# Kernel optimization log

Measured on AMD Instinct MI355X. Metric: run time of the kernel, lower is better.

Reference implementation:

```python
import jax, jax.numpy as jnp
import numpy as np


def _gcn_layer(x, W, b, row, col, num_nodes):
    # x: [N, F_in]; W: [F_in, F_out]; row/col: [E2] (with self-loops appended)
    xw = x @ W  # [N, F_out]
    ones = jnp.ones(row.shape[0], dtype=xw.dtype)
    deg = jax.ops.segment_sum(ones, col, num_segments=num_nodes)  # in-degree incl. self-loop
    dinv = jnp.where(deg > 0, jax.lax.rsqrt(deg), 0.0)
    norm = dinv[row] * dinv[col]  # [E2]
    msg = xw[row] * norm[:, None]  # gather + per-edge scale
    out = jax.ops.segment_sum(msg, col, num_segments=num_nodes)  # scatter-add to targets
    return out + b


def setup_inputs() -> dict:
    key = jax.random.key(0)
    k1, k2, k3, k4, k5 = jax.random.split(key, 5)
    N, E, F_in, F_hid = 100000, 640000, 128, 128
    x = jax.random.normal(k1, (N, F_in), dtype=jnp.float32)
    edge_index = jax.random.randint(k2, (2, E), 0, N, dtype=jnp.int64)
    # Glorot-style init like PyG GCNConv
    s1 = (6.0 / (F_in + F_hid)) ** 0.5
    W1 = jax.random.uniform(k3, (F_in, F_hid), jnp.float32, -s1, s1)
    b1 = jnp.zeros((F_hid,), jnp.float32)
    s2 = (6.0 / (F_hid + F_hid)) ** 0.5
    W2 = jax.random.uniform(k4, (F_hid, F_hid), jnp.float32, -s2, s2)
    b2 = jnp.zeros((F_hid,), jnp.float32)
    return {"x": x, "edge_index": edge_index, "W1": W1, "b1": b1, "W2": W2, "b2": b2}


def reference(x, edge_index, W1, b1, W2, b2):
    N = x.shape[0]
    # GCN adds self-loops before symmetric normalization (add_self_loops=True default)
    self_idx = jnp.arange(N, dtype=edge_index.dtype)
    row = jnp.concatenate([edge_index[0], self_idx])
    col = jnp.concatenate([edge_index[1], self_idx])
    h = _gcn_layer(x, W1, b1, row, col, N)
    h = jax.nn.relu(h)
    # dropout is identity in eval mode (training=False)
    out = _gcn_layer(h, W2, b2, row, col, N)
    return out
```

## Files before the change

kernel.cpp:

```cpp
#include <hip/hip_runtime.h>
#include <cstdint>
#include <cstddef>


typedef unsigned int u32;
typedef unsigned short u16;
typedef __attribute__((ext_vector_type(8))) short short8;
typedef __attribute__((ext_vector_type(4))) float f32x4;

__device__ __forceinline__ float bf2f(u32 lo16) {
  union { u32 u; float f; } c; c.u = lo16 << 16; return c.f;
}
__device__ __forceinline__ u32 f2bf(float f) {
  union { float f; u32 u; } c; c.f = f;
  return (c.u + 0x7fffu + ((c.u >> 16) & 1u)) >> 16;
}

__global__ __launch_bounds__(256) void zero_wt_kernel(
    const float* __restrict__ W1, const float* __restrict__ W2,
    u16* __restrict__ Wt1, u16* __restrict__ Wt2,
    u16* __restrict__ s1, u16* __restrict__ hp,
    int* __restrict__ cnt, int N) {
  int gt = blockIdx.x * 256 + threadIdx.x;
  if (gt < N) cnt[gt] = 0;
  if (gt < 32768) {
    const float* W = (gt < 16384) ? W1 : W2;
    u16* Wt = (gt < 16384) ? Wt1 : Wt2;
    int idx = gt & 16383;
    Wt[(idx & 127) * 128 + (idx >> 7)] = (u16)f2bf(W[idx]);
  }
  if (gt < 16) {
    ((uint4*)(s1 + (size_t)N * 128))[gt] = make_uint4(0, 0, 0, 0);
    ((uint4*)(hp + (size_t)N * 128))[gt] = make_uint4(0, 0, 0, 0);
  }
}

__global__ __launch_bounds__(256) void count_kernel(
    const int* __restrict__ cols, const int* __restrict__ rows,
    int* __restrict__ cnt, int E, int N) {
  int e = blockIdx.x * 256 + threadIdx.x;
  if (e >= E) return;
  int c = cols[e];
  int r = rows[e];
  if ((unsigned)c >= (unsigned)N || (unsigned)r >= (unsigned)N) return;
  atomicAdd(&cnt[c], 1);
}

__global__ __launch_bounds__(256) void scan1_kernel(
    const int* __restrict__ cnt, int* __restrict__ rowptr,
    int* __restrict__ bsum, float* __restrict__ dinv, int N) {
  __shared__ int sd[256];
  int t = threadIdx.x;
  int base = blockIdx.x * 1024 + t * 4;
  int c0 = (base + 0 < N) ? cnt[base + 0] : 0;
  int c1 = (base + 1 < N) ? cnt[base + 1] : 0;
  int c2 = (base + 2 < N) ? cnt[base + 2] : 0;
  int c3 = (base + 3 < N) ? cnt[base + 3] : 0;
  if (base + 0 < N) dinv[base + 0] = rsqrtf((float)c0 + 1.0f);
  if (base + 1 < N) dinv[base + 1] = rsqrtf((float)c1 + 1.0f);
  if (base + 2 < N) dinv[base + 2] = rsqrtf((float)c2 + 1.0f);
  if (base + 3 < N) dinv[base + 3] = rsqrtf((float)c3 + 1.0f);
  int s = c0 + c1 + c2 + c3;
  sd[t] = s;
  __syncthreads();
  for (int off = 1; off < 256; off <<= 1) {
    int v = (t >= off) ? sd[t - off] : 0;
    __syncthreads();
    sd[t] += v;
    __syncthreads();
  }
  int excl = sd[t] - s;
  if (base + 0 < N) rowptr[base + 0] = excl;
  if (base + 1 < N) rowptr[base + 1] = excl + c0;
  if (base + 2 < N) rowptr[base + 2] = excl + c0 + c1;
  if (base + 3 < N) rowptr[base + 3] = excl + c0 + c1 + c2;
  if (t == 255) bsum[blockIdx.x] = sd[255];
}

__global__ __launch_bounds__(128) void scan2_kernel(
    const int* __restrict__ bsum, int* __restrict__ bsum2,
    int* __restrict__ rowptr, int NB, int N) {
  __shared__ int sd[128];
  int t = threadIdx.x;
  int v = (t < NB) ? bsum[t] : 0;
  sd[t] = v;
  __syncthreads();
  for (int off = 1; off < 128; off <<= 1) {
    int u = (t >= off) ? sd[t - off] : 0;
    __syncthreads();
    sd[t] += u;
    __syncthreads();
  }
  bsum2[t] = sd[t] - v;
  if (t == NB - 1) rowptr[N] = sd[t];
}

__global__ __launch_bounds__(256) void finalize_kernel(
    const float* __restrict__ x, const float* __restrict__ dinv,
    int* __restrict__ rowptr, const int* __restrict__ bsum2,
    u16* __restrict__ s1, int N, int NB) {
  int b = blockIdx.x, t = threadIdx.x;
  if (b < NB) {
    int base = b * 1024 + t * 4;
    int add = bsum2[b];
#pragma unroll
    for (int k = 0; k < 4; k++)
      if (base + k < N) rowptr[base + k] += add;
  }
  int total = N * 16;
  for (int idx = b * 256 + t; idx < total; idx += gridDim.x * 256) {
    int node = idx >> 4, l = idx & 15;
    float di = dinv[node];
    const float* xp = x + (size_t)node * 128 + l * 8;
    float4 v0 = *(const float4*)xp;
    float4 v1 = *(const float4*)(xp + 4);
    uint4 p;
    p.x = f2bf(di * v0.x) | (f2bf(di * v0.y) << 16);
    p.y = f2bf(di * v0.z) | (f2bf(di * v0.w) << 16);
    p.z = f2bf(di * v1.x) | (f2bf(di * v1.y) << 16);
    p.w = f2bf(di * v1.z) | (f2bf(di * v1.w) << 16);
    ((uint4*)s1)[idx] = p;
  }
}

__global__ __launch_bounds__(256) void fill_kernel(
    const int* __restrict__ cols, const int* __restrict__ rows,
    const int* __restrict__ rowptr, int* __restrict__ cnt,
    int* __restrict__ adj, int E, int N) {
  int e = blockIdx.x * 256 + threadIdx.x;
  if (e >= E) return;
  int c = cols[e];
  int r = rows[e];
  if ((unsigned)c >= (unsigned)N || (unsigned)r >= (unsigned)N) return;
  int pos = atomicSub(&cnt[c], 1) - 1;
  if (pos >= 0) adj[rowptr[c] + pos] = r;
}

template <int LAYER>
__global__ __launch_bounds__(256) void fused_ag_kernel(
    const uint4* __restrict__ src, const int* __restrict__ rowptr,
    const int* __restrict__ adj, const float* __restrict__ dinv,
    const float* __restrict__ bias, const u16* __restrict__ Wt,
    void* __restrict__ out, int N) {
  __shared__ __align__(16) u16 Gs[64][136];
  __shared__ float dv_s[64];
  const int tid = threadIdx.x;
  const int row0 = blockIdx.x * 64;

  const int qw = tid >> 4;
  const int l = tid & 15;
#pragma unroll
  for (int pass = 0; pass < 4; ++pass) {
    int lrow = pass * 16 + qw;
    int node = row0 + lrow;
    float a[8] = {0.f, 0.f, 0.f, 0.f, 0.f, 0.f, 0.f, 0.f};
    float di = 0.f;
    if (node < N) {
      di = dinv[node];
      uint4 sv = src[(size_t)node * 16 + l];
      a[0] = bf2f(sv.x & 0xffff); a[1] = bf2f(sv.x >> 16);
      a[2] = bf2f(sv.y & 0xffff); a[3] = bf2f(sv.y >> 16);
      a[4] = bf2f(sv.z & 0xffff); a[5] = bf2f(sv.z >> 16);
      a[6] = bf2f(sv.w & 0xffff); a[7] = bf2f(sv.w >> 16);
      int beg = rowptr[node], end = rowptr[node + 1];
      for (int j = beg; j < end; j += 8) {
        int sidx[8];
#pragma unroll
        for (int k = 0; k < 8; k++) {
          int jj = j + k;
          sidx[k] = (jj < end) ? adj[jj] : N;
        }
        uint4 v[8];
#pragma unroll
        for (int k = 0; k < 8; k++) v[k] = src[(size_t)sidx[k] * 16 + l];
#pragma unroll
        for (int k = 0; k < 8; k++) {
          a[0] += bf2f(v[k].x & 0xffff); a[1] += bf2f(v[k].x >> 16);
          a[2] += bf2f(v[k].y & 0xffff); a[3] += bf2f(v[k].y >> 16);
          a[4] += bf2f(v[k].z & 0xffff); a[5] += bf2f(v[k].z >> 16);
          a[6] += bf2f(v[k].w & 0xffff); a[7] += bf2f(v[k].w >> 16);
        }
      }
    }
    uint4 p;
    p.x = f2bf(di * a[0]) | (f2bf(di * a[1]) << 16);
    p.y = f2bf(di * a[2]) | (f2bf(di * a[3]) << 16);
    p.z = f2bf(di * a[4]) | (f2bf(di * a[5]) << 16);
    p.w = f2bf(di * a[6]) | (f2bf(di * a[7]) << 16);
    *(uint4*)&Gs[lrow][l * 8] = p;
    if (l == 0) dv_s[lrow] = di;
  }
  __syncthreads();

  const int wave = tid >> 6, lane = tid & 63;
  const int lm = lane & 15, quad = lane >> 4;
  const int m0 = wave * 16;
  const u16* wbase = Wt + lm * 128 + quad * 8;
  f32x4 acc[8];
#pragma unroll
  for (int nt = 0; nt < 8; nt++) acc[nt] = (f32x4){0.f, 0.f, 0.f, 0.f};
#pragma unroll
  for (int k0 = 0; k0 < 128; k0 += 32) {
    short8 afrag = *(const short8*)&Gs[m0 + lm][k0 + quad * 8];
    short8 bfrag[8];
#pragma unroll
    for (int nt = 0; nt < 8; nt++)
      bfrag[nt] = *(const short8*)(wbase + nt * 2048 + k0);
#pragma unroll
    for (int nt = 0; nt < 8; nt++)
      acc[nt] = __builtin_amdgcn_mfma_f32_16x16x32_bf16(afrag, bfrag[nt], acc[nt], 0, 0, 0);
  }

  float bv[8];
#pragma unroll
  for (int nt = 0; nt < 8; nt++) bv[nt] = bias[nt * 16 + lm];

  if (LAYER == 1) {
    __syncthreads();
    int rbase = m0 + quad * 4;
#pragma unroll
    for (int r = 0; r < 4; r++) {
      int lrow = rbase + r;
      float dv = dv_s[lrow];
#pragma unroll
      for (int nt = 0; nt < 8; nt++) {
        float v = fmaxf(acc[nt][r] + bv[nt], 0.f);
        Gs[lrow][nt * 16 + lm] = (u16)f2bf(v * dv);
      }
    }
    __syncthreads();
    u16* C = (u16*)out;
#pragma unroll
    for (int i = 0; i < 4; i++) {
      int linear = tid + i * 256;
      int row = linear >> 4, c8 = linear & 15;
      int grow = row0 + row;
      if (grow < N)
        *(uint4*)(C + (size_t)grow * 128 + c8 * 8) = *(const uint4*)&Gs[row][c8 * 8];
    }
  } else {
    float* C = (float*)out;
#pragma unroll
    for (int r = 0; r < 4; r++) {
      int grow = row0 + m0 + quad * 4 + r;
      if (grow < N) {
        float* Cp = C + (size_t)grow * 128 + lm;
#pragma unroll
        for (int nt = 0; nt < 8; nt++)
          __builtin_nontemporal_store(acc[nt][r] + bv[nt], Cp + nt * 16);
      }
    }
  }
}

extern "C" void kernel_launch(void* const* d_in, const int* in_sizes, int n_in,
                              void* d_out, int out_size, void* d_ws, size_t ws_size,
                              hipStream_t stream) {
  const float* x  = (const float*)d_in[0];
  const int*   ei = (const int*)d_in[1];
  const float* W1 = (const float*)d_in[2];
  const float* b1 = (const float*)d_in[3];
  const float* W2 = (const float*)d_in[4];
  const float* b2 = (const float*)d_in[5];
  float* out = (float*)d_out;

  const int F = 128;
  const int N = in_sizes[0] / F;
  const int E = in_sizes[1] / 2;
  const int* rows = ei;
  const int* cols = ei + E;

  u16*   Wt1    = (u16*)d_ws;
  u16*   Wt2    = Wt1 + 128 * 128;
  u16*   s1     = Wt2 + 128 * 128;
  u16*   hp     = s1 + (size_t)(N + 1) * F;
  float* dinv   = (float*)(hp + (size_t)(N + 1) * F);
  int*   cnt    = (int*)(dinv + N);
  int*   rowptr = cnt + N;
  int*   adj    = rowptr + (N + 1);
  int*   bsum   = adj + E;
  int*   bsum2  = bsum + 128;

  const int NB = (N + 1023) / 1024;
  int eblocks = (E + 255) / 256;
  int nblocks = (N + 255) / 256;
  int fblocks = (NB > 784) ? NB : 784;

  zero_wt_kernel<<<nblocks, 256, 0, stream>>>(W1, W2, Wt1, Wt2, s1, hp, cnt, N);
  count_kernel<<<eblocks, 256, 0, stream>>>(cols, rows, cnt, E, N);
  scan1_kernel<<<NB, 256, 0, stream>>>(cnt, rowptr, bsum, dinv, N);
  scan2_kernel<<<1, 128, 0, stream>>>(bsum, bsum2, rowptr, NB, N);
  finalize_kernel<<<fblocks, 256, 0, stream>>>(x, dinv, rowptr, bsum2, s1, N, NB);
  fill_kernel<<<eblocks, 256, 0, stream>>>(cols, rows, rowptr, cnt, adj, E, N);

  int gblocks = (N + 63) / 64;
  fused_ag_kernel<1><<<gblocks, 256, 0, stream>>>(
      (const uint4*)s1, rowptr, adj, dinv, b1, Wt1, hp, N);
  fused_ag_kernel<2><<<gblocks, 256, 0, stream>>>(
      (const uint4*)hp, rowptr, adj, dinv, b2, Wt2, out, N);
}
```

Measured before the change: 281.8 us.

## Aggregate directly into MFMA fragments per wave, drop block-wide LDS staging

The gather-aggregate now maps each wave lane to a (node, k-chunk) pair that matches the MFMA A-fragment layout. Accumulated sums go straight into registers as bf16 fragments, which removes the shared-memory staging tile and the block-wide __syncthreads. Layer 2 output is now staged through per-wave LDS so rows are written as coalesced 16-byte nontemporal stores, and launch bounds request 4 blocks per CU. In exchange each lane holds 32 accumulators plus 16 in-flight uint4 loads, which raises register pressure. Each 16-lane group also touches only 4 of the 16 row chunks per load, which may reduce coalescing per instruction.

After: 355.7 us. 1.26x slower.

```diff
diff --git a/kernel.cpp b/kernel.cpp
--- a/kernel.cpp
+++ b/kernel.cpp
@@ -14,6 +14,12 @@
 __device__ __forceinline__ u32 f2bf(float f) {
   union { float f; u32 u; } c; c.f = f;
   return (c.u + 0x7fffu + ((c.u >> 16) & 1u)) >> 16;
+}
+__device__ __forceinline__ void acc8(float* a, uint4 v) {
+  a[0] += bf2f(v.x & 0xffff); a[1] += bf2f(v.x >> 16);
+  a[2] += bf2f(v.y & 0xffff); a[3] += bf2f(v.y >> 16);
+  a[4] += bf2f(v.z & 0xffff); a[5] += bf2f(v.z >> 16);
+  a[6] += bf2f(v.w & 0xffff); a[7] += bf2f(v.w >> 16);
 }
 
 __global__ __launch_bounds__(256) void zero_wt_kernel(
@@ -137,117 +143,119 @@
 }
 
 template <int LAYER>
-__global__ __launch_bounds__(256) void fused_ag_kernel(
-    const uint4* __restrict__ src, const int* __restrict__ rowptr,
+__global__ __launch_bounds__(256, 4) void fused_ag_kernel(
+    const u16* __restrict__ src, const int* __restrict__ rowptr,
     const int* __restrict__ adj, const float* __restrict__ dinv,
     const float* __restrict__ bias, const u16* __restrict__ Wt,
     void* __restrict__ out, int N) {
-  __shared__ __align__(16) u16 Gs[64][136];
-  __shared__ float dv_s[64];
+  __shared__ __align__(16) u16 Cs[4][16][136];
   const int tid = threadIdx.x;
-  const int row0 = blockIdx.x * 64;
-
-  const int qw = tid >> 4;
-  const int l = tid & 15;
-#pragma unroll
-  for (int pass = 0; pass < 4; ++pass) {
-    int lrow = pass * 16 + qw;
-    int node = row0 + lrow;
-    float a[8] = {0.f, 0.f, 0.f, 0.f, 0.f, 0.f, 0.f, 0.f};
-    float di = 0.f;
-    if (node < N) {
-      di = dinv[node];
-      uint4 sv = src[(size_t)node * 16 + l];
-      a[0] = bf2f(sv.x & 0xffff); a[1] = bf2f(sv.x >> 16);
-      a[2] = bf2f(sv.y & 0xffff); a[3] = bf2f(sv.y >> 16);
-      a[4] = bf2f(sv.z & 0xffff); a[5] = bf2f(sv.z >> 16);
-      a[6] = bf2f(sv.w & 0xffff); a[7] = bf2f(sv.w >> 16);
-      int beg = rowptr[node], end = rowptr[node + 1];
-      for (int j = beg; j < end; j += 8) {
-        int sidx[8];
-#pragma unroll
-        for (int k = 0; k < 8; k++) {
-          int jj = j + k;
-          sidx[k] = (jj < end) ? adj[jj] : N;
-        }
-        uint4 v[8];
-#pragma unroll
-        for (int k = 0; k < 8; k++) v[k] = src[(size_t)sidx[k] * 16 + l];
-#pragma unroll
-        for (int k = 0; k < 8; k++) {
-          a[0] += bf2f(v[k].x & 0xffff); a[1] += bf2f(v[k].x >> 16);
-          a[2] += bf2f(v[k].y & 0xffff); a[3] += bf2f(v[k].y >> 16);
-          a[4] += bf2f(v[k].z & 0xffff); a[5] += bf2f(v[k].z >> 16);
-          a[6] += bf2f(v[k].w & 0xffff); a[7] += bf2f(v[k].w >> 16);
-        }
+  const int wave = tid >> 6, lane = tid & 63;
+  const int lm = lane & 15, quad = lane >> 4;
+  const int wrow0 = blockIdx.x * 64 + wave * 16;
+  const int node = wrow0 + lm;
+
+  float a[4][8];
+#pragma unroll
+  for (int s = 0; s < 4; s++)
+#pragma unroll
+    for (int e = 0; e < 8; e++) a[s][e] = 0.f;
+  float di = 0.f;
+  if (node < N) {
+    di = dinv[node];
+    const uint4* srow = (const uint4*)src + (size_t)node * 16 + quad;
+    uint4 sv[4];
+#pragma unroll
+    for (int s = 0; s < 4; s++) sv[s] = srow[s * 4];
+#pragma unroll
+    for (int s = 0; s < 4; s++) acc8(a[s], sv[s]);
+
+    int beg = rowptr[node], end = rowptr[node + 1];
+    for (int j = beg; j < end; j += 4) {
+      int sidx[4];
+#pragma unroll
+      for (int k = 0; k < 4; k++) {
+        int jj = j + k;
+        sidx[k] = (jj < end) ? adj[jj] : N;
+      }
+      uint4 v[4][4];
+#pragma unroll
+      for (int k = 0; k < 4; k++) {
+        const uint4* p = (const uint4*)src + (size_t)sidx[k] * 16 + quad;
+#pragma unroll
+        for (int s = 0; s < 4; s++) v[k][s] = p[s * 4];
+      }
+#pragma unroll
+      for (int k = 0; k < 4; k++)
+#pragma unroll
+        for (int s = 0; s < 4; s++) acc8(a[s], v[k][s]);
+    }
+  }
+
+  short8 afrag[4];
+#pragma unroll
+  for (int s = 0; s < 4; s++)
+#pragma unroll
+    for (int e = 0; e < 8; e++) afrag[s][e] = (short)f2bf(di * a[s][e]);
+
+  const u16* wbase = Wt + lm * 128 + quad * 8;
+  f32x4 macc[8];
+#pragma unroll
+  for (int nt = 0; nt < 8; nt++) macc[nt] = (f32x4){0.f, 0.f, 0.f, 0.f};
+#pragma unroll
+  for (int s = 0; s < 4; s++) {
+    short8 bf[8];
+#pragma unroll
+    for (int nt = 0; nt < 8; nt++)
+      bf[nt] = *(const short8*)(wbase + nt * 2048 + s * 32);
+#pragma unroll
+    for (int nt = 0; nt < 8; nt++)
+      macc[nt] = __builtin_amdgcn_mfma_f32_16x16x32_bf16(afrag[s], bf[nt], macc[nt], 0, 0, 0);
+  }
+
+  float bv[8];
+#pragma unroll
+  for (int nt = 0; nt < 8; nt++) bv[nt] = bias[nt * 16 + lm];
+
+  if (LAYER == 1) {
+    u16 (*cs)[136] = Cs[wave];
+#pragma unroll
+    for (int r = 0; r < 4; r++) {
+      float dv = __shfl(di, quad * 4 + r);
+#pragma unroll
+      for (int nt = 0; nt < 8; nt++) {
+        float v = fmaxf(macc[nt][r] + bv[nt], 0.f);
+        cs[quad * 4 + r][nt * 16 + lm] = (u16)f2bf(v * dv);
       }
     }
-    uint4 p;
-    p.x = f2bf(di * a[0]) | (f2bf(di * a[1]) << 16);
-    p.y = f2bf(di * a[2]) | (f2bf(di * a[3]) << 16);
-    p.z = f2bf(di * a[4]) | (f2bf(di * a[5]) << 16);
-    p.w = f2bf(di * a[6]) | (f2bf(di * a[7]) << 16);
-    *(uint4*)&Gs[lrow][l * 8] = p;
-    if (l == 0) dv_s[lrow] = di;
-  }
-  __syncthreads();
-
-  const int wave = tid >> 6, lane = tid & 63;
-  const int lm = lane & 15, quad = lane >> 4;
-  const int m0 = wave * 16;
-  const u16* wbase = Wt + lm * 128 + quad * 8;
-  f32x4 acc[8];
-#pragma unroll
-  for (int nt = 0; nt < 8; nt++) acc[nt] = (f32x4){0.f, 0.f, 0.f, 0.f};
-#pragma unroll
-  for (int k0 = 0; k0 < 128; k0 += 32) {
-    short8 afrag = *(const short8*)&Gs[m0 + lm][k0 + quad * 8];
-    short8 bfrag[8];
-#pragma unroll
-    for (int nt = 0; nt < 8; nt++)
-      bfrag[nt] = *(const short8*)(wbase + nt * 2048 + k0);
-#pragma unroll
-    for (int nt = 0; nt < 8; nt++)
-      acc[nt] = __builtin_amdgcn_mfma_f32_16x16x32_bf16(afrag, bfrag[nt], acc[nt], 0, 0, 0);
-  }
-
-  float bv[8];
-#pragma unroll
-  for (int nt = 0; nt < 8; nt++) bv[nt] = bias[nt * 16 + lm];
-
-  if (LAYER == 1) {
-    __syncthreads();
-    int rbase = m0 + quad * 4;
-#pragma unroll
-    for (int r = 0; r < 4; r++) {
-      int lrow = rbase + r;
-      float dv = dv_s[lrow];
-#pragma unroll
-      for (int nt = 0; nt < 8; nt++) {
-        float v = fmaxf(acc[nt][r] + bv[nt], 0.f);
-        Gs[lrow][nt * 16 + lm] = (u16)f2bf(v * dv);
-      }
-    }
-    __syncthreads();
     u16* C = (u16*)out;
 #pragma unroll
     for (int i = 0; i < 4; i++) {
-      int linear = tid + i * 256;
+      int linear = lane + i * 64;
       int row = linear >> 4, c8 = linear & 15;
-      int grow = row0 + row;
+      int grow = wrow0 + row;
       if (grow < N)
-        *(uint4*)(C + (size_t)grow * 128 + c8 * 8) = *(const uint4*)&Gs[row][c8 * 8];
+        *(uint4*)(C + (size_t)grow * 128 + c8 * 8) = *(const uint4*)&cs[row][c8 * 8];
     }
   } else {
+    float (*fs)[68] = (float(*)[68])Cs[wave];
     float* C = (float*)out;
 #pragma unroll
-    for (int r = 0; r < 4; r++) {
-      int grow = row0 + m0 + quad * 4 + r;
-      if (grow < N) {
-        float* Cp = C + (size_t)grow * 128 + lm;
-#pragma unroll
-        for (int nt = 0; nt < 8; nt++)
-          __builtin_nontemporal_store(acc[nt][r] + bv[nt], Cp + nt * 16);
+    for (int p = 0; p < 2; p++) {
+#pragma unroll
+      for (int r = 0; r < 4; r++)
+#pragma unroll
+        for (int t = 0; t < 4; t++)
+          fs[quad * 4 + r][t * 16 + lm] = macc[p * 4 + t][r] + bv[p * 4 + t];
+#pragma unroll
+      for (int i = 0; i < 4; i++) {
+        int linear = lane + i * 64;
+        int row = linear >> 4, c4 = linear & 15;
+        int grow = wrow0 + row;
+        if (grow < N) {
+          f32x4 v = *(const f32x4*)&fs[row][c4 * 4];
+          __builtin_nontemporal_store(v, (f32x4*)(C + (size_t)grow * 128 + p * 64 + c4 * 4));
+        }
       }
     }
   }
@@ -295,7 +303,7 @@
 
   int gblocks = (N + 63) / 64;
   fused_ag_kernel<1><<<gblocks, 256, 0, stream>>>(
-      (const uint4*)s1, rowptr, adj, dinv, b1, Wt1, hp, N);
+      s1, rowptr, adj, dinv, b1, Wt1, hp, N);
   fused_ag_kernel<2><<<gblocks, 256, 0, stream>>>(
-      (const uint4*)hp, rowptr, adj, dinv, b2, Wt2, out, N);
-}
+      hp, rowptr, adj, dinv, b2, Wt2, out, N);
+}
```
